# Performance work log

Measured on AMD Instinct MI355X. Metric: run time of the kernel, lower is better.

The kernel has to match this reference:

```python
import jax, jax.numpy as jnp
import numpy as np
import math

H = 128
NUM_RBF = 32
CUTOFF_UPPER = 4.5
CUTOFF_LOWER = 0.0
N_NODES = 16384
N_EDGES = 65536
EPS = 1e-5


def _layernorm(x, gamma, beta):
    m = x.mean(-1, keepdims=True)
    v = ((x - m) ** 2).mean(-1, keepdims=True)
    return (x - m) / jnp.sqrt(v + EPS) * gamma + beta


def _cosine_cutoff(d):
    # cutoff_lower == 0 branch of CosineCutoff
    return 0.5 * (jnp.cos(d * (math.pi / CUTOFF_UPPER)) + 1.0) * (d < CUTOFF_UPPER).astype(d.dtype)


def _expnorm_rbf(d):
    alpha = 5.0 / (CUTOFF_UPPER - CUTOFF_LOWER)
    start = math.exp(-CUTOFF_UPPER + CUTOFF_LOWER)
    means = jnp.linspace(start, 1.0, NUM_RBF, dtype=d.dtype)
    betas = jnp.full((NUM_RBF,), (2.0 / NUM_RBF * (1.0 - start)) ** -2, dtype=d.dtype)
    de = d[:, None]
    return _cosine_cutoff(de) * jnp.exp(-betas * (jnp.exp(alpha * (-de + CUTOFF_LOWER)) - means) ** 2)


def _skew(v):  # [E,3] -> [E,3,3]
    z = jnp.zeros(v.shape[0], v.dtype)
    return jnp.stack([z, -v[:, 2], v[:, 1], v[:, 2], z, -v[:, 0], -v[:, 1], v[:, 0], z], axis=1).reshape(-1, 3, 3)


def _sym(v):  # traceless symmetric part of outer product, [E,3] -> [E,3,3]
    M = v[:, :, None] * v[:, None, :]
    tr3 = (v * v).sum(-1)[:, None, None] / 3.0
    return M - tr3 * jnp.eye(3, dtype=v.dtype)


def _tensor_norm(T):  # [...,3,3] -> [...]
    return (T ** 2).sum((-2, -1))


def setup_inputs() -> dict:
    key = jax.random.key(0)
    ks = jax.random.split(key, 32)
    s = 0.05
    inp = {
        'z': jax.random.randint(ks[0], (N_NODES,), 0, 128, dtype=jnp.int32),
        'pos': jax.random.normal(ks[1], (N_NODES, 3), jnp.float32) * 3.0,
        'batch': jnp.zeros((N_NODES,), jnp.int32),
        'edge_index': jax.random.randint(ks[2], (2, N_EDGES), 0, N_NODES, dtype=jnp.int64),
        'emb_w': jax.random.normal(ks[3], (128, H), jnp.float32) * s,
        'emb2_w': jax.random.normal(ks[4], (H, 2 * H), jnp.float32) * s,
        'emb2_b': jnp.zeros((H,), jnp.float32),
        'dp1_w': jax.random.normal(ks[5], (H, NUM_RBF), jnp.float32) * s,
        'dp1_b': jnp.zeros((H,), jnp.float32),
        'dp2_w': jax.random.normal(ks[6], (H, NUM_RBF), jnp.float32) * s,
        'dp2_b': jnp.zeros((H,), jnp.float32),
        'dp3_w': jax.random.normal(ks[7], (H, NUM_RBF), jnp.float32) * s,
        'dp3_b': jnp.zeros((H,), jnp.float32),
        'lt0_w': jax.random.normal(ks[8], (H, H), jnp.float32) * s,
        'lt1_w': jax.random.normal(ks[9], (H, H), jnp.float32) * s,
        'lt2_w': jax.random.normal(ks[10], (H, H), jnp.float32) * s,
        'ls0_w': jax.random.normal(ks[11], (2 * H, H), jnp.float32) * s,
        'ls0_b': jnp.zeros((2 * H,), jnp.float32),
        'ls1_w': jax.random.normal(ks[12], (3 * H, 2 * H), jnp.float32) * s,
        'ls1_b': jnp.zeros((3 * H,), jnp.float32),
        'in_gamma': jnp.ones((H,), jnp.float32),
        'in_beta': jnp.zeros((H,), jnp.float32),
        'lin_w': jax.random.normal(ks[13], (H, 3 * H), jnp.float32) * s,
        'lin_b': jnp.zeros((H,), jnp.float32),
        'on_gamma': jnp.ones((3 * H,), jnp.float32),
        'on_beta': jnp.zeros((3 * H,), jnp.float32),
        'ol1_w': jax.random.normal(ks[14], (H // 2, H), jnp.float32) * s,
        'ol1_b': jnp.zeros((H // 2,), jnp.float32),
        'ol2_w': jax.random.normal(ks[15], (1, H // 2), jnp.float32) * s,
        'ol2_b': jnp.zeros((1,), jnp.float32),
    }
    return inp


def reference(z, pos, batch, edge_index, emb_w, emb2_w, emb2_b, dp1_w, dp1_b, dp2_w, dp2_b,
              dp3_w, dp3_b, lt0_w, lt1_w, lt2_w, ls0_w, ls0_b, ls1_w, ls1_b,
              in_gamma, in_beta, lin_w, lin_b, on_gamma, on_beta, ol1_w, ol1_b, ol2_w, ol2_b):
    src, dst = edge_index[0], edge_index[1]
    edge_vec = pos[src] - pos[dst]                            # [E,3]
    edge_weight = jnp.sqrt((edge_vec ** 2).sum(-1))           # [E]
    edge_attr = _expnorm_rbf(edge_weight)                     # [E,R]
    self_mask = src == dst
    edge_vec_norm = edge_vec / jnp.where(self_mask, 1.0, edge_weight)[:, None]

    # atomic-number message: Zij = emb2(concat(emb[z_src], emb[z_dst]))
    Zemb = emb_w[z]                                           # [N,H]
    Zcat = jnp.concatenate([Zemb[src], Zemb[dst]], axis=-1)   # [E,2H]
    Zij = Zcat @ emb2_w.T + emb2_b                            # [E,H]

    C = (_cosine_cutoff(edge_weight)[:, None] * Zij)[:, :, None, None]  # [E,H,1,1]
    eye = jnp.eye(3, dtype=pos.dtype)[None, None]
    d1 = (edge_attr @ dp1_w.T + dp1_b)[:, :, None, None]      # [E,H,1,1]
    d2 = (edge_attr @ dp2_w.T + dp2_b)[:, :, None, None]
    d3 = (edge_attr @ dp3_w.T + dp3_b)[:, :, None, None]
    Iij = d1 * C * eye                                        # [E,H,3,3]
    Aij = d2 * C * _skew(edge_vec_norm)[:, None, :, :]
    Sij = d3 * C * _sym(edge_vec_norm)[:, None, :, :]

    N = pos.shape[0]
    I0 = jax.ops.segment_sum(Iij, src, num_segments=N)        # [N,H,3,3]
    A0 = jax.ops.segment_sum(Aij, src, num_segments=N)
    S0 = jax.ops.segment_sum(Sij, src, num_segments=N)

    tnorm = _layernorm(_tensor_norm(I0 + A0 + S0), in_gamma, in_beta)  # [N,H]
    nrm = jax.nn.silu(tnorm @ ls0_w.T + ls0_b)
    nrm = jax.nn.silu(nrm @ ls1_w.T + ls1_b).reshape(-1, H, 3)          # [N,H,3]

    I = jnp.einsum('nhij,kh->nkij', I0, lt0_w) * nrm[:, :, 0, None, None]
    A = jnp.einsum('nhij,kh->nkij', A0, lt1_w) * nrm[:, :, 1, None, None]
    S = jnp.einsum('nhij,kh->nkij', S0, lt2_w) * nrm[:, :, 2, None, None]

    x = jnp.concatenate([_tensor_norm(I), _tensor_norm(A), _tensor_norm(S)], axis=-1)  # [N,3H]
    x = _layernorm(x, on_gamma, on_beta)
    x = jax.nn.silu(x @ lin_w.T + lin_b)                       # [N,H]
    x = jax.nn.silu(x @ ol1_w.T + ol1_b)                       # [N,H//2]
    y = x @ ol2_w.T + ol2_b                                    # [N,1] per-atom scalar
    return y
```

## Files before the change

### kernel.cpp

```cpp
#include <hip/hip_runtime.h>
#include <math.h>

#define NN 16384
#define NE 65536
#define HH 128

constexpr double D_START = 0.011108996538242306;
constexpr double D_STEP  = (1.0 - D_START) / 31.0;
constexpr float  F_ALPHA = (float)(5.0/4.5);
constexpr double D_BB    = (2.0/32.0)*(1.0 - D_START);
constexpr float  F_BETA  = (float)(1.0/(D_BB*D_BB));
constexpr float  F_PIC   = (float)(M_PI/4.5);

#define POOL_BYTES (16u*1024u*1024u)
__device__ __align__(256) static char g_pool[POOL_BYTES];

typedef __attribute__((ext_vector_type(8))) short bf16x8;
typedef __attribute__((ext_vector_type(4))) float f32x4;

__device__ __forceinline__ float siluf(float x){
  return x * (1.0f/(1.0f + expf(-x)));
}
__device__ __forceinline__ short f2bf(float x){
  unsigned u = __float_as_uint(x);
  unsigned r = (u + 0x7fffu + ((u>>16)&1u)) >> 16;
  return (short)r;
}
__device__ __forceinline__ float bf2f(short h){
  return __uint_as_float(((unsigned)(unsigned short)h)<<16);
}
__device__ __forceinline__ void split_bf(float x, short& h, short& l){
  h = f2bf(x);
  l = f2bf(x - bf2f(h));
}

__global__ __launch_bounds__(256) void k_prep(
    const int* __restrict__ ei, const float* __restrict__ pos,
    const int* __restrict__ z,
    const float* __restrict__ emb_w, const float* __restrict__ emb2_w,
    const float* __restrict__ emb2_b,
    const float* __restrict__ ls0, const float* __restrict__ ls1,
    const float* __restrict__ lin, const float* __restrict__ lt0,
    const float* __restrict__ lt1, const float* __restrict__ lt2,
    const float* __restrict__ dp1, const float* __restrict__ dp2,
    const float* __restrict__ dp3, const float* __restrict__ ol1,
    float* __restrict__ PZ, float* __restrict__ QZ,
    int* __restrict__ bcnt, int* __restrict__ bucket,
    int* __restrict__ ezs, int* __restrict__ ezd, float* __restrict__ ev,
    short* __restrict__ atth, short* __restrict__ attl,
    short* __restrict__ ls0h, short* __restrict__ ls0l,
    short* __restrict__ ls1h, short* __restrict__ ls1l,
    short* __restrict__ linh, short* __restrict__ linl,
    short* __restrict__ lt0h, short* __restrict__ lt0l,
    short* __restrict__ lt1h, short* __restrict__ lt1l,
    short* __restrict__ lt2h, short* __restrict__ lt2l,
    short* __restrict__ dwh, short* __restrict__ dwl,
    short* __restrict__ ol1h, short* __restrict__ ol1l){
  int b = blockIdx.x;
  if (b < 64){
    __shared__ float erow[2][128];
    int sub = threadIdx.x >> 7, h = threadIdx.x & 127;
    int a = b*2 + sub;
    erow[sub][h] = emb_w[a*128 + h];
    __syncthreads();
    float p = 0.f, q = 0.f;
    #pragma unroll 8
    for (int k=0;k<128;++k){
      float e = erow[sub][k];
      p += e * emb2_w[h*256 + k];
      q += e * emb2_w[h*256 + 128 + k];
    }
    PZ[a*128 + h] = p + emb2_b[h];
    QZ[a*128 + h] = q;
    return;
  }
  if (b < 1040){
    int tid = (b-64)*256 + threadIdx.x;
    const float* s; short *dh, *dl; int i;
    if      (tid < 32768)  { s=ls0; dh=ls0h; dl=ls0l; i=tid; }
    else if (tid < 131072) { s=ls1; dh=ls1h; dl=ls1l; i=tid-32768; }
    else if (tid < 180224) { s=lin; dh=linh; dl=linl; i=tid-131072; }
    else if (tid < 196608) { s=lt0; dh=lt0h; dl=lt0l; i=tid-180224; }
    else if (tid < 212992) { s=lt1; dh=lt1h; dl=lt1l; i=tid-196608; }
    else if (tid < 229376) { s=lt2; dh=lt2h; dl=lt2l; i=tid-212992; }
    else if (tid < 241664) {
      int j = tid - 229376;
      int g = j >> 12, idx = j & 4095;
      s = (g==0)?dp1:((g==1)?dp2:dp3);
      short h,l; split_bf(s[idx], h, l);
      dwh[j] = h; dwl[j] = l;
      return;
    }
    else { s=ol1; dh=ol1h; dl=ol1l; i=tid-241664; }
    short h,l; split_bf(s[i], h, l);
    dh[i] = h; dl[i] = l;
    return;
  }
  {
    int e = (b-1040)*256 + threadIdx.x;
    int s = ei[e];
    int t = ei[NE + e];
    float dx = pos[3*s+0] - pos[3*t+0];
    float dy = pos[3*s+1] - pos[3*t+1];
    float dz = pos[3*s+2] - pos[3*t+2];
    float d = sqrtf(dx*dx + dy*dy + dz*dz);
    if (d < 4.5f){
      int g16 = s >> 4;
      int p = atomicAdd(&bcnt[g16], 1);
      if (p < 512) bucket[g16*512 + p] = (e<<4) | (s & 15);
      ezs[e] = z[s];
      ezd[e] = z[t];
      float denom = (s==t) ? 1.0f : d;
      ev[4*e+0] = dx/denom;
      ev[4*e+1] = dy/denom;
      ev[4*e+2] = dz/denom;
      float cut = 0.5f*(cosf(d*F_PIC) + 1.0f);
      ev[4*e+3] = cut;
      float q = expf(-F_ALPHA*d);
      #pragma unroll
      for (int r=0;r<32;++r){
        float m = (float)(D_START + r*D_STEP);
        float u = q - m;
        float a = cut * expf(-F_BETA*u*u);
        short hh, ll; split_bf(a, hh, ll);
        atth[32*e + r] = hh;
        attl[32*e + r] = ll;
      }
    }
  }
}

__global__ __launch_bounds__(256, 2) void k_mega(
    const int* __restrict__ bcnt, const int* __restrict__ bucket,
    const int* __restrict__ ezs, const int* __restrict__ ezd,
    const float* __restrict__ ev,
    const short* __restrict__ atth, const short* __restrict__ attl,
    const short* __restrict__ dwh, const short* __restrict__ dwl,
    const float* __restrict__ db1, const float* __restrict__ db2,
    const float* __restrict__ db3,
    const float* __restrict__ PZ, const float* __restrict__ QZ,
    const float* __restrict__ in_g, const float* __restrict__ in_b,
    const short* __restrict__ w0h, const short* __restrict__ w0l,
    const short* __restrict__ w1h, const short* __restrict__ w1l,
    const short* __restrict__ w2h, const short* __restrict__ w2l,
    const short* __restrict__ ls0h, const short* __restrict__ ls0l,
    const float* __restrict__ ls0b,
    const short* __restrict__ ls1h, const short* __restrict__ ls1l,
    const float* __restrict__ ls1b,
    const short* __restrict__ linh, const short* __restrict__ linl,
    const float* __restrict__ linb,
    const short* __restrict__ ol1h, const short* __restrict__ ol1l,
    const float* __restrict__ ol1b,
    const float* __restrict__ ol2w, const float* __restrict__ ol2b,
    const float* __restrict__ on_g, const float* __restrict__ on_b,
    float* __restrict__ y){
  __shared__ __align__(16) char sm[76288];
  float* Dt    = (float*)sm;
  int*   elocal= (int*)(sm + 24832);
  int*   lcnt  = (int*)(sm + 26880);
  int*   loff  = lcnt + 16;
  int*   lcur  = loff + 17;
  short* T1h   = (short*)sm;
  short* T1l   = (short*)(sm + 9216);
  short* PlnL  = (short*)sm;
  float* xls   = (float*)sm;
  short* X3h   = (short*)sm;
  short* X3l   = (short*)(sm + 5120);
  float* partL = (float*)(sm + 10240);
  int*   tmpb  = (int*)(sm + 51200);
  short* tnhL  = (short*)(sm + 51200);
  short* tnlL  = (short*)(sm + 51200 + 5120);
  float* NRMt  = (float*)(sm + 51200);
  short* xhL   = (short*)(sm + 51200);
  short* xlL   = (short*)(sm + 51200 + 12544);

  int t = threadIdx.x;
  int b = blockIdx.x;
  int w = t >> 6, lane = t & 63;
  int col16 = lane & 15, quad = lane >> 4;
  int bn = b*16;
  int node = t >> 4, q = t & 15;

  int ecnt = bcnt[b]; if (ecnt > 512) ecnt = 512;
  if (t < 16){ lcnt[t] = 0; lcur[t] = 0; }
  __syncthreads();
  for (int j = t; j < ecnt; j += 256){
    int val = bucket[b*512 + j];
    tmpb[j] = val;
    atomicAdd(&lcnt[val & 15], 1);
  }
  __syncthreads();
  if (t == 0){
    int a = 0;
    #pragma unroll
    for (int i=0;i<16;++i){ loff[i] = a; a += lcnt[i]; }
    loff[16] = a;
  }
  __syncthreads();
  for (int j = t; j < ecnt; j += 256){
    int val = tmpb[j];
    int nd = val & 15;
    int p = loff[nd] + atomicAdd(&lcur[nd], 1);
    elocal[p] = val >> 4;
  }
  __syncthreads();
  int etot = loff[16];
  int e0n = loff[node], e1n = loff[node+1];

  float pv[10][8];
  #pragma unroll
  for (int p=0;p<10;++p)
    #pragma unroll
    for (int i=0;i<8;++i) pv[p][i]=0.f;

  const float* dbp[3] = {db1, db2, db3};
  for (int c0 = 0; c0 < etot; c0 += 16){
    int jA = c0 + col16; if (jA >= etot) jA = etot - 1;
    int eA = elocal[jA];
    bf16x8 ah = *(const bf16x8*)(atth + (size_t)eA*32 + quad*8);
    bf16x8 al = *(const bf16x8*)(attl + (size_t)eA*32 + quad*8);
    f32x4 dacc[6];
    #pragma unroll
    for (int nt=0;nt<6;++nt) dacc[nt] = (f32x4){0.f,0.f,0.f,0.f};
    #pragma unroll
    for (int nt=0;nt<6;++nt){
      int col = w*96 + nt*16 + col16;
      int g = col >> 7, cg = col & 127;
      bf16x8 wh = *(const bf16x8*)(dwh + g*4096 + cg*32 + quad*8);
      bf16x8 wl = *(const bf16x8*)(dwl + g*4096 + cg*32 + quad*8);
      dacc[nt] = __builtin_amdgcn_mfma_f32_16x16x32_bf16(ah, wh, dacc[nt], 0,0,0);
      dacc[nt] = __builtin_amdgcn_mfma_f32_16x16x32_bf16(ah, wl, dacc[nt], 0,0,0);
      dacc[nt] = __builtin_amdgcn_mfma_f32_16x16x32_bf16(al, wh, dacc[nt], 0,0,0);
    }
    #pragma unroll
    for (int nt=0;nt<6;++nt){
      int col = w*96 + nt*16 + col16;
      int g = col >> 7;
      float bb = dbp[g][col & 127];
      #pragma unroll
      for (int r=0;r<4;++r)
        Dt[(quad*4+r)*388 + col] = dacc[nt][r] + bb;
    }
    __syncthreads();
    int jlo = e0n > c0 ? e0n : c0;
    int jhi0 = c0 + 16; if (jhi0 > etot) jhi0 = etot;
    int jhi = e1n < jhi0 ? e1n : jhi0;
    for (int j = jlo; j < jhi; ++j){
      int le = j - c0;
      int e = elocal[j];
      float4 evv = *(const float4*)(ev + 4*e);
      int zs = ezs[e], zd = ezd[e];
      const float* pz = PZ + zs*128 + q*8;
      const float* qz = QZ + zd*128 + q*8;
      const float* dr = Dt + le*388 + q*8;
      float vx = evv.x, vy = evv.y, vz = evv.z, cut = evv.w;
      float t3v = (vx*vx + vy*vy + vz*vz)*(1.0f/3.0f);
      #pragma unroll
      for (int i=0;i<8;++i){
        float C = cut * (pz[i] + qz[i]);
        float d1 = dr[i], d2 = dr[128+i], d3 = dr[256+i];
        pv[0][i] += d1*C;
        float wa = d2*C;
        pv[1][i] += wa*vx; pv[2][i] += wa*vy; pv[3][i] += wa*vz;
        float ws = d3*C;
        pv[4][i] += ws*(vx*vx - t3v);
        pv[5][i] += ws*(vy*vy - t3v);
        pv[6][i] += ws*(vz*vz - t3v);
        pv[7][i] += ws*(vx*vy);
        pv[8][i] += ws*(vx*vz);
        pv[9][i] += ws*(vy*vz);
      }
    }
    __syncthreads();
  }

  {
    float tnv[8];
    float s8 = 0.f;
    #pragma unroll
    for (int i=0;i<8;++i){
      float x = 3.f*pv[0][i]*pv[0][i]
              + 2.f*(pv[1][i]*pv[1][i]+pv[2][i]*pv[2][i]+pv[3][i]*pv[3][i])
              + (pv[4][i]*pv[4][i]+pv[5][i]*pv[5][i]+pv[6][i]*pv[6][i])
              + 2.f*(pv[7][i]*pv[7][i]+pv[8][i]*pv[8][i]+pv[9][i]*pv[9][i]);
      tnv[i] = x; s8 += x;
    }
    #pragma unroll
    for (int o=8;o;o>>=1) s8 += __shfl_xor(s8, o, 64);
    float mean = s8*(1.0f/128.0f);
    float vq = 0.f;
    #pragma unroll
    for (int i=0;i<8;++i){ float d = tnv[i]-mean; vq += d*d; }
    #pragma unroll
    for (int o=8;o;o>>=1) vq += __shfl_xor(vq, o, 64);
    float rstd = 1.0f/sqrtf(vq*(1.0f/128.0f) + 1e-5f);
    #pragma unroll
    for (int i=0;i<8;++i){
      int h = q*8 + i;
      float val = (tnv[i]-mean)*rstd*in_g[h] + in_b[h];
      short hh, ll; split_bf(val, hh, ll);
      tnhL[node*160 + h] = hh;
      tnlL[node*160 + h] = ll;
    }
  }
  __syncthreads();

  {
    f32x4 macc[4];
    #pragma unroll
    for (int nt=0;nt<4;++nt) macc[nt] = (f32x4){0.f,0.f,0.f,0.f};
    #pragma unroll
    for (int kc=0; kc<4; ++kc){
      bf16x8 tah = *(const bf16x8*)(tnhL + col16*160 + kc*32 + quad*8);
      bf16x8 tal = *(const bf16x8*)(tnlL + col16*160 + kc*32 + quad*8);
      #pragma unroll
      for (int nt=0;nt<4;++nt){
        int n = w*64 + nt*16 + col16;
        bf16x8 wh = *(const bf16x8*)(ls0h + n*128 + kc*32 + quad*8);
        bf16x8 wl = *(const bf16x8*)(ls0l + n*128 + kc*32 + quad*8);
        macc[nt] = __builtin_amdgcn_mfma_f32_16x16x32_bf16(tah, wh, macc[nt], 0,0,0);
        macc[nt] = __builtin_amdgcn_mfma_f32_16x16x32_bf16(tah, wl, macc[nt], 0,0,0);
        macc[nt] = __builtin_amdgcn_mfma_f32_16x16x32_bf16(tal, wh, macc[nt], 0,0,0);
      }
    }
    #pragma unroll
    for (int nt=0;nt<4;++nt){
      int n = w*64 + nt*16 + col16;
      float bb = ls0b[n];
      #pragma unroll
      for (int r=0;r<4;++r){
        float v = siluf(macc[nt][r] + bb);
        short hh, ll; split_bf(v, hh, ll);
        T1h[(quad*4+r)*288 + n] = hh;
        T1l[(quad*4+r)*288 + n] = ll;
      }
    }
    __syncthreads();
    f32x4 nacc[6];
    #pragma unroll
    for (int nt=0;nt<6;++nt) nacc[nt] = (f32x4){0.f,0.f,0.f,0.f};
    #pragma unroll
    for (int kc=0; kc<8; ++kc){
      bf16x8 tah = *(const bf16x8*)(T1h + col16*288 + kc*32 + quad*8);
      bf16x8 tal = *(const bf16x8*)(T1l + col16*288 + kc*32 + quad*8);
      #pragma unroll
      for (int nt=0;nt<6;++nt){
        int n = w*96 + nt*16 + col16;
        bf16x8 wh = *(const bf16x8*)(ls1h + n*256 + kc*32 + quad*8);
        bf16x8 wl = *(const bf16x8*)(ls1l + n*256 + kc*32 + quad*8);
        nacc[nt] = __builtin_amdgcn_mfma_f32_16x16x32_bf16(tah, wh, nacc[nt], 0,0,0);
        nacc[nt] = __builtin_amdgcn_mfma_f32_16x16x32_bf16(tah, wl, nacc[nt], 0,0,0);
        nacc[nt] = __builtin_amdgcn_mfma_f32_16x16x32_bf16(tal, wh, nacc[nt], 0,0,0);
      }
    }
    __syncthreads();
    #pragma unroll
    for (int nt=0;nt<6;++nt){
      int n = w*96 + nt*16 + col16;
      float bb = ls1b[n];
      #pragma unroll
      for (int r=0;r<4;++r)
        NRMt[(quad*4+r)*388 + n] = siluf(nacc[nt][r] + bb);
    }
  }

  const short* wgh[3] = {w0h, w1h, w2h};
  const short* wgl[3] = {w0l, w1l, w2l};
  float xI[2][4], xA[2][4], xS[2][4];
  #pragma unroll
  for (int tt=0;tt<2;++tt)
    #pragma unroll
    for (int r=0;r<4;++r){ xI[tt][r]=0.f; xA[tt][r]=0.f; xS[tt][r]=0.f; }
  #pragma unroll
  for (int pass=0; pass<2; ++pass){
    const int pbase = pass*5;
    __syncthreads();
    #pragma unroll
    for (int pl=0; pl<5; ++pl){
      short* dst = PlnL + (pl*4 + (q>>2))*1280 + node*80 + (q&3)*16;
      #pragma unroll
      for (int i=0;i<8;++i){
        short hh, ll; split_bf(pv[pbase+pl][i], hh, ll);
        dst[i] = hh; dst[8+i] = ll;
      }
    }
    __syncthreads();
    f32x4 acc[5][2];
    #pragma unroll
    for (int pl=0;pl<5;++pl)
      #pragma unroll
      for (int tt=0;tt<2;++tt) acc[pl][tt] = (f32x4){0.f,0.f,0.f,0.f};
    #pragma unroll
    for (int hc4=0; hc4<4; ++hc4){
      bf16x8 bh[2], bl[2];
      int curg = -1;
      #pragma unroll
      for (int pl=0; pl<5; ++pl){
        const int p = pbase + pl;
        const int g = (p==0)?0:((p<4)?1:2);
        if (g != curg){
          #pragma unroll
          for (int tt=0; tt<2; ++tt){
            int row = w*32 + tt*16 + col16;
            bh[tt] = *(const bf16x8*)(wgh[g] + row*128 + hc4*32 + quad*8);
            bl[tt] = *(const bf16x8*)(wgl[g] + row*128 + hc4*32 + quad*8);
          }
          curg = g;
        }
        const short* ab = PlnL + (pl*4 + hc4)*1280 + col16*80 + quad*16;
        bf16x8 ah = *(const bf16x8*)(ab);
        bf16x8 al = *(const bf16x8*)(ab + 8);
        #pragma unroll
        for (int tt=0; tt<2; ++tt){
          acc[pl][tt] = __builtin_amdgcn_mfma_f32_16x16x32_bf16(ah, bh[tt], acc[pl][tt], 0,0,0);
          acc[pl][tt] = __builtin_amdgcn_mfma_f32_16x16x32_bf16(ah, bl[tt], acc[pl][tt], 0,0,0);
          acc[pl][tt] = __builtin_amdgcn_mfma_f32_16x16x32_bf16(al, bh[tt], acc[pl][tt], 0,0,0);
        }
      }
    }
    #pragma unroll
    for (int pl=0; pl<5; ++pl){
      const int p = pbase + pl;
      const int sel = (p==0)?0:((p<4)?1:2);
      #pragma unroll
      for (int tt=0; tt<2; ++tt){
        int k = w*32 + tt*16 + col16;
        #pragma unroll
        for (int r=0; r<4; ++r){
          int nloc = quad*4 + r;
          float n = NRMt[nloc*388 + 3*k + sel];
          float v = acc[pl][tt][r]*n;
          if (p==0)      xI[tt][r]  = 3.f*v*v;
          else if (p<4)  xA[tt][r] += 2.f*v*v;
          else if (p<7)  xS[tt][r] += v*v;
          else           xS[tt][r] += 2.f*v*v;
        }
      }
    }
  }
  __syncthreads();

  #pragma unroll
  for (int tt=0; tt<2; ++tt){
    int k = w*32 + tt*16 + col16;
    #pragma unroll
    for (int r=0; r<4; ++r){
      int nloc = quad*4 + r;
      xls[nloc*388 + k]       = xI[tt][r];
      xls[nloc*388 + 128 + k] = xA[tt][r];
      xls[nloc*388 + 256 + k] = xS[tt][r];
    }
  }
  __syncthreads();
  {
    float vv[24];
    float s = 0.f;
    #pragma unroll
    for (int i=0;i<24;++i){ vv[i] = xls[node*388 + q*24 + i]; s += vv[i]; }
    #pragma unroll
    for (int o=8;o;o>>=1) s += __shfl_xor(s, o, 64);
    float mean = s*(1.0f/384.0f);
    float qsum = 0.f;
    #pragma unroll
    for (int i=0;i<24;++i){ float d = vv[i]-mean; qsum += d*d; }
    #pragma unroll
    for (int o=8;o;o>>=1) qsum += __shfl_xor(qsum, o, 64);
    float rstd = 1.0f/sqrtf(qsum*(1.0f/384.0f) + 1e-5f);
    #pragma unroll
    for (int i=0;i<24;++i){
      int c = q*24 + i;
      float val = (vv[i]-mean)*rstd*on_g[c] + on_b[c];
      short hh, ll; split_bf(val, hh, ll);
      xhL[node*392 + c] = hh;
      xlL[node*392 + c] = ll;
    }
  }
  __syncthreads();

  {
    f32x4 lacc[2];
    #pragma unroll
    for (int nt=0;nt<2;++nt) lacc[nt] = (f32x4){0.f,0.f,0.f,0.f};
    #pragma unroll
    for (int kc=0; kc<12; ++kc){
      bf16x8 xah = *(const bf16x8*)(xhL + col16*392 + kc*32 + quad*8);
      bf16x8 xal = *(const bf16x8*)(xlL + col16*392 + kc*32 + quad*8);
      #pragma unroll
      for (int nt=0;nt<2;++nt){
        int n = w*32 + nt*16 + col16;
        bf16x8 wh = *(const bf16x8*)(linh + n*384 + kc*32 + quad*8);
        bf16x8 wl = *(const bf16x8*)(linl + n*384 + kc*32 + quad*8);
        lacc[nt] = __builtin_amdgcn_mfma_f32_16x16x32_bf16(xah, wh, lacc[nt], 0,0,0);
        lacc[nt] = __builtin_amdgcn_mfma_f32_16x16x32_bf16(xah, wl, lacc[nt], 0,0,0);
        lacc[nt] = __builtin_amdgcn_mfma_f32_16x16x32_bf16(xal, wh, lacc[nt], 0,0,0);
      }
    }
    __syncthreads();
    #pragma unroll
    for (int nt=0;nt<2;++nt){
      int n = w*32 + nt*16 + col16;
      float bb = linb[n];
      #pragma unroll
      for (int r=0;r<4;++r){
        float v = siluf(lacc[nt][r] + bb);
        short hh, ll; split_bf(v, hh, ll);
        X3h[(quad*4+r)*160 + n] = hh;
        X3l[(quad*4+r)*160 + n] = ll;
      }
    }
    __syncthreads();
  }

  {
    f32x4 hacc = (f32x4){0.f,0.f,0.f,0.f};
    int n = w*16 + col16;
    #pragma unroll
    for (int kc=0; kc<4; ++kc){
      bf16x8 xah = *(const bf16x8*)(X3h + col16*160 + kc*32 + quad*8);
      bf16x8 xal = *(const bf16x8*)(X3l + col16*160 + kc*32 + quad*8);
      bf16x8 wh = *(const bf16x8*)(ol1h + n*128 + kc*32 + quad*8);
      bf16x8 wl = *(const bf16x8*)(ol1l + n*128 + kc*32 + quad*8);
      hacc = __builtin_amdgcn_mfma_f32_16x16x32_bf16(xah, wh, hacc, 0,0,0);
      hacc = __builtin_amdgcn_mfma_f32_16x16x32_bf16(xah, wl, hacc, 0,0,0);
      hacc = __builtin_amdgcn_mfma_f32_16x16x32_bf16(xal, wh, hacc, 0,0,0);
    }
    float b1 = ol1b[n], w2 = ol2w[n];
    #pragma unroll
    for (int r=0;r<4;++r){
      float v = siluf(hacc[r] + b1) * w2;
      #pragma unroll
      for (int o=8;o;o>>=1) v += __shfl_xor(v, o, 64);
      if (col16 == 0) partL[w*16 + quad*4 + r] = v;
    }
    __syncthreads();
    if (t < 16)
      y[bn + t] = partL[t] + partL[16+t] + partL[32+t] + partL[48+t] + ol2b[0];
  }
}

extern "C" void kernel_launch(void* const* d_in, const int* in_sizes, int n_in,
                              void* d_out, int out_size, void* d_ws, size_t ws_size,
                              hipStream_t stream) {
  const int*   z      = (const int*)d_in[0];
  const float* pos    = (const float*)d_in[1];
  const int*   ei     = (const int*)d_in[3];
  const float* emb_w  = (const float*)d_in[4];
  const float* emb2_w = (const float*)d_in[5];
  const float* emb2_b = (const float*)d_in[6];
  const float* dp1_w  = (const float*)d_in[7];
  const float* dp1_b  = (const float*)d_in[8];
  const float* dp2_w  = (const float*)d_in[9];
  const float* dp2_b  = (const float*)d_in[10];
  const float* dp3_w  = (const float*)d_in[11];
  const float* dp3_b  = (const float*)d_in[12];
  const float* lt0_w  = (const float*)d_in[13];
  const float* lt1_w  = (const float*)d_in[14];
  const float* lt2_w  = (const float*)d_in[15];
  const float* ls0_w  = (const float*)d_in[16];
  const float* ls0_b  = (const float*)d_in[17];
  const float* ls1_w  = (const float*)d_in[18];
  const float* ls1_b  = (const float*)d_in[19];
  const float* in_g   = (const float*)d_in[20];
  const float* in_b   = (const float*)d_in[21];
  const float* lin_w  = (const float*)d_in[22];
  const float* lin_b  = (const float*)d_in[23];
  const float* on_g   = (const float*)d_in[24];
  const float* on_b   = (const float*)d_in[25];
  const float* ol1_w  = (const float*)d_in[26];
  const float* ol1_b  = (const float*)d_in[27];
  const float* ol2_w  = (const float*)d_in[28];
  const float* ol2_b  = (const float*)d_in[29];
  float* out = (float*)d_out;

  const size_t NEED = 14u*1024u*1024u;
  char* wsb = (char*)d_ws;
  if (ws_size < NEED){
    void* p = nullptr;
    hipGetSymbolAddress(&p, HIP_SYMBOL(g_pool));
    wsb = (char*)p;
  }
  size_t off = 0;
  auto alloc = [&](size_t bytes)->void*{
    void* p = wsb + off;
    off = (off + bytes + 255) & ~(size_t)255;
    return p;
  };
  float* PZ      = (float*)alloc(128*128*4);
  float* QZ      = (float*)alloc(128*128*4);
  int*   bcnt    = (int*)  alloc(1024*4);
  int*   bucket  = (int*)  alloc((size_t)1024*512*4);
  int*   ezs     = (int*)  alloc(NE*4);
  int*   ezd     = (int*)  alloc(NE*4);
  float* ev      = (float*)alloc((size_t)NE*4*4);
  short* atth    = (short*)alloc((size_t)NE*32*2);
  short* attl    = (short*)alloc((size_t)NE*32*2);
  short* dwh     = (short*)alloc(3*128*32*2);
  short* dwl     = (short*)alloc(3*128*32*2);
  short* ls0h    = (short*)alloc(256*128*2);
  short* ls0l    = (short*)alloc(256*128*2);
  short* ls1h    = (short*)alloc(384*256*2);
  short* ls1l    = (short*)alloc(384*256*2);
  short* linh    = (short*)alloc(128*384*2);
  short* linl    = (short*)alloc(128*384*2);
  short* lt0h    = (short*)alloc(128*128*2);
  short* lt0l    = (short*)alloc(128*128*2);
  short* lt1h    = (short*)alloc(128*128*2);
  short* lt1l    = (short*)alloc(128*128*2);
  short* lt2h    = (short*)alloc(128*128*2);
  short* lt2l    = (short*)alloc(128*128*2);
  short* ol1h    = (short*)alloc(64*128*2);
  short* ol1l    = (short*)alloc(64*128*2);

  hipMemsetAsync(bcnt, 0, 1024*4, stream);

  k_prep<<<1296, 256, 0, stream>>>(ei, pos, z, emb_w, emb2_w, emb2_b,
                                   ls0_w, ls1_w, lin_w, lt0_w, lt1_w, lt2_w,
                                   dp1_w, dp2_w, dp3_w, ol1_w,
                                   PZ, QZ, bcnt, bucket, ezs, ezd, ev, atth, attl,
                                   ls0h, ls0l, ls1h, ls1l, linh, linl,
                                   lt0h, lt0l, lt1h, lt1l, lt2h, lt2l,
                                   dwh, dwl, ol1h, ol1l);
  k_mega<<<NN/16, 256, 0, stream>>>(bcnt, bucket, ezs, ezd, ev, atth, attl,
                                    dwh, dwl, dp1_b, dp2_b, dp3_b,
                                    PZ, QZ, in_g, in_b,
                                    lt0h, lt0l, lt1h, lt1l, lt2h, lt2l,
                                    ls0h, ls0l, ls0_b, ls1h, ls1l, ls1_b,
                                    linh, linl, lin_b, ol1h, ol1l, ol1_b,
                                    ol2_w, ol2_b, on_g, on_b, out);
}
```

Baseline: 266.9 us.

## Double k_mega block size to 512 threads, halving per-thread work

Raises the fused per-node kernel from 256 to 512 threads per block (8 waves), with 32 threads per node each owning 4 hidden channels instead of 8. All MFMA tile loops are re-split so each wave handles half as many output tiles. The aim is fewer registers per thread and more waves to hide the latency of gathers and MFMAs. The cost is more barrier participants, wider shuffle reductions, and possible LDS pressure limiting the requested 4 blocks per CU.

Result: no change. 264.8 us (median of 2 runs) (-0.8%).

```diff
diff --git a/kernel.cpp b/kernel.cpp
--- a/kernel.cpp
+++ b/kernel.cpp
@@ -130,7 +130,7 @@
   }
 }
 
-__global__ __launch_bounds__(256, 2) void k_mega(
+__global__ __launch_bounds__(512, 4) void k_mega(
     const int* __restrict__ bcnt, const int* __restrict__ bucket,
     const int* __restrict__ ezs, const int* __restrict__ ezd,
     const float* __restrict__ ev,
@@ -179,12 +179,12 @@
   int w = t >> 6, lane = t & 63;
   int col16 = lane & 15, quad = lane >> 4;
   int bn = b*16;
-  int node = t >> 4, q = t & 15;
+  int node = t >> 5, q5 = t & 31;
 
   int ecnt = bcnt[b]; if (ecnt > 512) ecnt = 512;
   if (t < 16){ lcnt[t] = 0; lcur[t] = 0; }
   __syncthreads();
-  for (int j = t; j < ecnt; j += 256){
+  for (int j = t; j < ecnt; j += 512){
     int val = bucket[b*512 + j];
     tmpb[j] = val;
     atomicAdd(&lcnt[val & 15], 1);
@@ -197,7 +197,7 @@
     loff[16] = a;
   }
   __syncthreads();
-  for (int j = t; j < ecnt; j += 256){
+  for (int j = t; j < ecnt; j += 512){
     int val = tmpb[j];
     int nd = val & 15;
     int p = loff[nd] + atomicAdd(&lcur[nd], 1);
@@ -207,11 +207,11 @@
   int etot = loff[16];
   int e0n = loff[node], e1n = loff[node+1];
 
-  float pv[10][8];
+  float pv[10][4];
   #pragma unroll
   for (int p=0;p<10;++p)
     #pragma unroll
-    for (int i=0;i<8;++i) pv[p][i]=0.f;
+    for (int i=0;i<4;++i) pv[p][i]=0.f;
 
   const float* dbp[3] = {db1, db2, db3};
   for (int c0 = 0; c0 < etot; c0 += 16){
@@ -219,12 +219,12 @@
     int eA = elocal[jA];
     bf16x8 ah = *(const bf16x8*)(atth + (size_t)eA*32 + quad*8);
     bf16x8 al = *(const bf16x8*)(attl + (size_t)eA*32 + quad*8);
-    f32x4 dacc[6];
-    #pragma unroll
-    for (int nt=0;nt<6;++nt) dacc[nt] = (f32x4){0.f,0.f,0.f,0.f};
-    #pragma unroll
-    for (int nt=0;nt<6;++nt){
-      int col = w*96 + nt*16 + col16;
+    f32x4 dacc[3];
+    #pragma unroll
+    for (int nt=0;nt<3;++nt) dacc[nt] = (f32x4){0.f,0.f,0.f,0.f};
+    #pragma unroll
+    for (int nt=0;nt<3;++nt){
+      int col = w*48 + nt*16 + col16;
       int g = col >> 7, cg = col & 127;
       bf16x8 wh = *(const bf16x8*)(dwh + g*4096 + cg*32 + quad*8);
       bf16x8 wl = *(const bf16x8*)(dwl + g*4096 + cg*32 + quad*8);
@@ -233,8 +233,8 @@
       dacc[nt] = __builtin_amdgcn_mfma_f32_16x16x32_bf16(al, wh, dacc[nt], 0,0,0);
     }
     #pragma unroll
-    for (int nt=0;nt<6;++nt){
-      int col = w*96 + nt*16 + col16;
+    for (int nt=0;nt<3;++nt){
+      int col = w*48 + nt*16 + col16;
       int g = col >> 7;
       float bb = dbp[g][col & 127];
       #pragma unroll
@@ -245,18 +245,19 @@
     int jlo = e0n > c0 ? e0n : c0;
     int jhi0 = c0 + 16; if (jhi0 > etot) jhi0 = etot;
     int jhi = e1n < jhi0 ? e1n : jhi0;
+    int h0 = q5*4;
     for (int j = jlo; j < jhi; ++j){
       int le = j - c0;
       int e = elocal[j];
       float4 evv = *(const float4*)(ev + 4*e);
       int zs = ezs[e], zd = ezd[e];
-      const float* pz = PZ + zs*128 + q*8;
-      const float* qz = QZ + zd*128 + q*8;
-      const float* dr = Dt + le*388 + q*8;
+      const float* pz = PZ + zs*128 + h0;
+      const float* qz = QZ + zd*128 + h0;
+      const float* dr = Dt + le*388 + h0;
       float vx = evv.x, vy = evv.y, vz = evv.z, cut = evv.w;
       float t3v = (vx*vx + vy*vy + vz*vz)*(1.0f/3.0f);
       #pragma unroll
-      for (int i=0;i<8;++i){
+      for (int i=0;i<4;++i){
         float C = cut * (pz[i] + qz[i]);
         float d1 = dr[i], d2 = dr[128+i], d3 = dr[256+i];
         pv[0][i] += d1*C;
@@ -275,10 +276,10 @@
   }
 
   {
-    float tnv[8];
+    float tnv[4];
     float s8 = 0.f;
     #pragma unroll
-    for (int i=0;i<8;++i){
+    for (int i=0;i<4;++i){
       float x = 3.f*pv[0][i]*pv[0][i]
               + 2.f*(pv[1][i]*pv[1][i]+pv[2][i]*pv[2][i]+pv[3][i]*pv[3][i])
               + (pv[4][i]*pv[4][i]+pv[5][i]*pv[5][i]+pv[6][i]*pv[6][i])
@@ -286,17 +287,17 @@
       tnv[i] = x; s8 += x;
     }
     #pragma unroll
-    for (int o=8;o;o>>=1) s8 += __shfl_xor(s8, o, 64);
+    for (int o=16;o;o>>=1) s8 += __shfl_xor(s8, o, 64);
     float mean = s8*(1.0f/128.0f);
     float vq = 0.f;
     #pragma unroll
-    for (int i=0;i<8;++i){ float d = tnv[i]-mean; vq += d*d; }
-    #pragma unroll
-    for (int o=8;o;o>>=1) vq += __shfl_xor(vq, o, 64);
+    for (int i=0;i<4;++i){ float d = tnv[i]-mean; vq += d*d; }
+    #pragma unroll
+    for (int o=16;o;o>>=1) vq += __shfl_xor(vq, o, 64);
     float rstd = 1.0f/sqrtf(vq*(1.0f/128.0f) + 1e-5f);
     #pragma unroll
-    for (int i=0;i<8;++i){
-      int h = q*8 + i;
+    for (int i=0;i<4;++i){
+      int h = q5*4 + i;
       float val = (tnv[i]-mean)*rstd*in_g[h] + in_b[h];
       short hh, ll; split_bf(val, hh, ll);
       tnhL[node*160 + h] = hh;
@@ -306,16 +307,16 @@
   __syncthreads();
 
   {
-    f32x4 macc[4];
-    #pragma unroll
-    for (int nt=0;nt<4;++nt) macc[nt] = (f32x4){0.f,0.f,0.f,0.f};
+    f32x4 macc[2];
+    #pragma unroll
+    for (int nt=0;nt<2;++nt) macc[nt] = (f32x4){0.f,0.f,0.f,0.f};
     #pragma unroll
     for (int kc=0; kc<4; ++kc){
       bf16x8 tah = *(const bf16x8*)(tnhL + col16*160 + kc*32 + quad*8);
       bf16x8 tal = *(const bf16x8*)(tnlL + col16*160 + kc*32 + quad*8);
       #pragma unroll
-      for (int nt=0;nt<4;++nt){
-        int n = w*64 + nt*16 + col16;
+      for (int nt=0;nt<2;++nt){
+        int n = w*32 + nt*16 + col16;
         bf16x8 wh = *(const bf16x8*)(ls0h + n*128 + kc*32 + quad*8);
         bf16x8 wl = *(const bf16x8*)(ls0l + n*128 + kc*32 + quad*8);
         macc[nt] = __builtin_amdgcn_mfma_f32_16x16x32_bf16(tah, wh, macc[nt], 0,0,0);
@@ -324,8 +325,8 @@
       }
     }
     #pragma unroll
-    for (int nt=0;nt<4;++nt){
-      int n = w*64 + nt*16 + col16;
+    for (int nt=0;nt<2;++nt){
+      int n = w*32 + nt*16 + col16;
       float bb = ls0b[n];
       #pragma unroll
       for (int r=0;r<4;++r){
@@ -336,16 +337,16 @@
       }
     }
     __syncthreads();
-    f32x4 nacc[6];
-    #pragma unroll
-    for (int nt=0;nt<6;++nt) nacc[nt] = (f32x4){0.f,0.f,0.f,0.f};
+    f32x4 nacc[3];
+    #pragma unroll
+    for (int nt=0;nt<3;++nt) nacc[nt] = (f32x4){0.f,0.f,0.f,0.f};
     #pragma unroll
     for (int kc=0; kc<8; ++kc){
       bf16x8 tah = *(const bf16x8*)(T1h + col16*288 + kc*32 + quad*8);
       bf16x8 tal = *(const bf16x8*)(T1l + col16*288 + kc*32 + quad*8);
       #pragma unroll
-      for (int nt=0;nt<6;++nt){
-        int n = w*96 + nt*16 + col16;
+      for (int nt=0;nt<3;++nt){
+        int n = w*48 + nt*16 + col16;
         bf16x8 wh = *(const bf16x8*)(ls1h + n*256 + kc*32 + quad*8);
         bf16x8 wl = *(const bf16x8*)(ls1l + n*256 + kc*32 + quad*8);
         nacc[nt] = __builtin_amdgcn_mfma_f32_16x16x32_bf16(tah, wh, nacc[nt], 0,0,0);
@@ -355,8 +356,8 @@
     }
     __syncthreads();
     #pragma unroll
-    for (int nt=0;nt<6;++nt){
-      int n = w*96 + nt*16 + col16;
+    for (int nt=0;nt<3;++nt){
+      int n = w*48 + nt*16 + col16;
       float bb = ls1b[n];
       #pragma unroll
       for (int r=0;r<4;++r)
@@ -366,109 +367,95 @@
 
   const short* wgh[3] = {w0h, w1h, w2h};
   const short* wgl[3] = {w0l, w1l, w2l};
-  float xI[2][4], xA[2][4], xS[2][4];
+  float xI[4], xA[4], xS[4];
   #pragma unroll
-  for (int tt=0;tt<2;++tt)
-    #pragma unroll
-    for (int r=0;r<4;++r){ xI[tt][r]=0.f; xA[tt][r]=0.f; xS[tt][r]=0.f; }
+  for (int r=0;r<4;++r){ xI[r]=0.f; xA[r]=0.f; xS[r]=0.f; }
   #pragma unroll
   for (int pass=0; pass<2; ++pass){
     const int pbase = pass*5;
     __syncthreads();
     #pragma unroll
     for (int pl=0; pl<5; ++pl){
-      short* dst = PlnL + (pl*4 + (q>>2))*1280 + node*80 + (q&3)*16;
-      #pragma unroll
-      for (int i=0;i<8;++i){
+      short* dst = PlnL + (pl*4 + (q5>>3))*1280 + node*80 + ((q5>>1)&3)*16 + (q5&1)*4;
+      #pragma unroll
+      for (int i=0;i<4;++i){
         short hh, ll; split_bf(pv[pbase+pl][i], hh, ll);
         dst[i] = hh; dst[8+i] = ll;
       }
     }
     __syncthreads();
-    f32x4 acc[5][2];
-    #pragma unroll
-    for (int pl=0;pl<5;++pl)
-      #pragma unroll
-      for (int tt=0;tt<2;++tt) acc[pl][tt] = (f32x4){0.f,0.f,0.f,0.f};
+    f32x4 acc[5];
+    #pragma unroll
+    for (int pl=0;pl<5;++pl) acc[pl] = (f32x4){0.f,0.f,0.f,0.f};
     #pragma unroll
     for (int hc4=0; hc4<4; ++hc4){
-      bf16x8 bh[2], bl[2];
+      bf16x8 bh, bl;
       int curg = -1;
       #pragma unroll
       for (int pl=0; pl<5; ++pl){
         const int p = pbase + pl;
         const int g = (p==0)?0:((p<4)?1:2);
         if (g != curg){
-          #pragma unroll
-          for (int tt=0; tt<2; ++tt){
-            int row = w*32 + tt*16 + col16;
-            bh[tt] = *(const bf16x8*)(wgh[g] + row*128 + hc4*32 + quad*8);
-            bl[tt] = *(const bf16x8*)(wgl[g] + row*128 + hc4*32 + quad*8);
-          }
+          int row = w*16 + col16;
+          bh = *(const bf16x8*)(wgh[g] + row*128 + hc4*32 + quad*8);
+          bl = *(const bf16x8*)(wgl[g] + row*128 + hc4*32 + quad*8);
           curg = g;
         }
         const short* ab = PlnL + (pl*4 + hc4)*1280 + col16*80 + quad*16;
         bf16x8 ah = *(const bf16x8*)(ab);
         bf16x8 al = *(const bf16x8*)(ab + 8);
-        #pragma unroll
-        for (int tt=0; tt<2; ++tt){
-          acc[pl][tt] = __builtin_amdgcn_mfma_f32_16x16x32_bf16(ah, bh[tt], acc[pl][tt], 0,0,0);
-          acc[pl][tt] = __builtin_amdgcn_mfma_f32_16x16x32_bf16(ah, bl[tt], acc[pl][tt], 0,0,0);
-          acc[pl][tt] = __builtin_amdgcn_mfma_f32_16x16x32_bf16(al, bh[tt], acc[pl][tt], 0,0,0);
-        }
+        acc[pl] = __builtin_amdgcn_mfma_f32_16x16x32_bf16(ah, bh, acc[pl], 0,0,0);
+        acc[pl] = __builtin_amdgcn_mfma_f32_16x16x32_bf16(ah, bl, acc[pl], 0,0,0);
+        acc[pl] = __builtin_amdgcn_mfma_f32_16x16x32_bf16(al, bh, acc[pl], 0,0,0);
       }
     }
     #pragma unroll
     for (int pl=0; pl<5; ++pl){
       const int p = pbase + pl;
       const int sel = (p==0)?0:((p<4)?1:2);
-      #pragma unroll
-      for (int tt=0; tt<2; ++tt){
-        int k = w*32 + tt*16 + col16;
-        #pragma unroll
-        for (int r=0; r<4; ++r){
-          int nloc = quad*4 + r;
-          float n = NRMt[nloc*388 + 3*k + sel];
-          float v = acc[pl][tt][r]*n;
-          if (p==0)      xI[tt][r]  = 3.f*v*v;
-          else if (p<4)  xA[tt][r] += 2.f*v*v;
-          else if (p<7)  xS[tt][r] += v*v;
-          else           xS[tt][r] += 2.f*v*v;
-        }
-      }
-    }
-  }
-  __syncthreads();
-
-  #pragma unroll
-  for (int tt=0; tt<2; ++tt){
-    int k = w*32 + tt*16 + col16;
+      int k = w*16 + col16;
+      #pragma unroll
+      for (int r=0; r<4; ++r){
+        int nloc = quad*4 + r;
+        float n = NRMt[nloc*388 + 3*k + sel];
+        float v = acc[pl][r]*n;
+        if (p==0)      xI[r]  = 3.f*v*v;
+        else if (p<4)  xA[r] += 2.f*v*v;
+        else if (p<7)  xS[r] += v*v;
+        else           xS[r] += 2.f*v*v;
+      }
+    }
+  }
+  __syncthreads();
+
+  {
+    int k = w*16 + col16;
     #pragma unroll
     for (int r=0; r<4; ++r){
       int nloc = quad*4 + r;
-      xls[nloc*388 + k]       = xI[tt][r];
-      xls[nloc*388 + 128 + k] = xA[tt][r];
-      xls[nloc*388 + 256 + k] = xS[tt][r];
+      xls[nloc*388 + k]       = xI[r];
+      xls[nloc*388 + 128 + k] = xA[r];
+      xls[nloc*388 + 256 + k] = xS[r];
     }
   }
   __syncthreads();
   {
-    float vv[24];
+    float vv[12];
     float s = 0.f;
     #pragma unroll
-    for (int i=0;i<24;++i){ vv[i] = xls[node*388 + q*24 + i]; s += vv[i]; }
-    #pragma unroll
-    for (int o=8;o;o>>=1) s += __shfl_xor(s, o, 64);
+    for (int i=0;i<12;++i){ vv[i] = xls[node*388 + q5*12 + i]; s += vv[i]; }
+    #pragma unroll
+    for (int o=16;o;o>>=1) s += __shfl_xor(s, o, 64);
     float mean = s*(1.0f/384.0f);
     float qsum = 0.f;
     #pragma unroll
-    for (int i=0;i<24;++i){ float d = vv[i]-mean; qsum += d*d; }
-    #pragma unroll
-    for (int o=8;o;o>>=1) qsum += __shfl_xor(qsum, o, 64);
+    for (int i=0;i<12;++i){ float d = vv[i]-mean; qsum += d*d; }
+    #pragma unroll
+    for (int o=16;o;o>>=1) qsum += __shfl_xor(qsum, o, 64);
     float rstd = 1.0f/sqrtf(qsum*(1.0f/384.0f) + 1e-5f);
     #pragma unroll
-    for (int i=0;i<24;++i){
-      int c = q*24 + i;
+    for (int i=0;i<12;++i){
+      int c = q5*12 + i;
       float val = (vv[i]-mean)*rstd*on_g[c] + on_b[c];
       short hh, ll; split_bf(val, hh, ll);
       xhL[node*392 + c] = hh;
@@ -478,40 +465,31 @@
   __syncthreads();
 
   {
-    f32x4 lacc[2];
-    #pragma unroll
-    for (int nt=0;nt<2;++nt) lacc[nt] = (f32x4){0.f,0.f,0.f,0.f};
+    f32x4 lacc = (f32x4){0.f,0.f,0.f,0.f};
+    int n = w*16 + col16;
     #pragma unroll
     for (int kc=0; kc<12; ++kc){
       bf16x8 xah = *(const bf16x8*)(xhL + col16*392 + kc*32 + quad*8);
       bf16x8 xal = *(const bf16x8*)(xlL + col16*392 + kc*32 + quad*8);
-      #pragma unroll
-      for (int nt=0;nt<2;++nt){
-        int n = w*32 + nt*16 + col16;
-        bf16x8 wh = *(const bf16x8*)(linh + n*384 + kc*32 + quad*8);
-        bf16x8 wl = *(const bf16x8*)(linl + n*384 + kc*32 + quad*8);
-        lacc[nt] = __builtin_amdgcn_mfma_f32_16x16x32_bf16(xah, wh, lacc[nt], 0,0,0);
-        lacc[nt] = __builtin_amdgcn_mfma_f32_16x16x32_bf16(xah, wl, lacc[nt], 0,0,0);
-        lacc[nt] = __builtin_amdgcn_mfma_f32_16x16x32_bf16(xal, wh, lacc[nt], 0,0,0);
-      }
-    }
-    __syncthreads();
-    #pragma unroll
-    for (int nt=0;nt<2;++nt){
-      int n = w*32 + nt*16 + col16;
-      float bb = linb[n];
-      #pragma unroll
-      for (int r=0;r<4;++r){
-        float v = siluf(lacc[nt][r] + bb);
-        short hh, ll; split_bf(v, hh, ll);
-        X3h[(quad*4+r)*160 + n] = hh;
-        X3l[(quad*4+r)*160 + n] = ll;
-      }
-    }
-    __syncthreads();
-  }
-
-  {
+      bf16x8 wh = *(const bf16x8*)(linh + n*384 + kc*32 + quad*8);
+      bf16x8 wl = *(const bf16x8*)(linl + n*384 + kc*32 + quad*8);
+      lacc = __builtin_amdgcn_mfma_f32_16x16x32_bf16(xah, wh, lacc, 0,0,0);
+      lacc = __builtin_amdgcn_mfma_f32_16x16x32_bf16(xah, wl, lacc, 0,0,0);
+      lacc = __builtin_amdgcn_mfma_f32_16x16x32_bf16(xal, wh, lacc, 0,0,0);
+    }
+    __syncthreads();
+    float bb = linb[n];
+    #pragma unroll
+    for (int r=0;r<4;++r){
+      float v = siluf(lacc[r] + bb);
+      short hh, ll; split_bf(v, hh, ll);
+      X3h[(quad*4+r)*160 + n] = hh;
+      X3l[(quad*4+r)*160 + n] = ll;
+    }
+    __syncthreads();
+  }
+
+  if (w < 4){
     f32x4 hacc = (f32x4){0.f,0.f,0.f,0.f};
     int n = w*16 + col16;
     #pragma unroll
@@ -532,10 +510,10 @@
       for (int o=8;o;o>>=1) v += __shfl_xor(v, o, 64);
       if (col16 == 0) partL[w*16 + quad*4 + r] = v;
     }
-    __syncthreads();
-    if (t < 16)
-      y[bn + t] = partL[t] + partL[16+t] + partL[32+t] + partL[48+t] + ol2b[0];
-  }
+  }
+  __syncthreads();
+  if (t < 16)
+    y[bn + t] = partL[t] + partL[16+t] + partL[32+t] + partL[48+t] + ol2b[0];
 }
 
 extern "C" void kernel_launch(void* const* d_in, const int* in_sizes, int n_in,
@@ -620,7 +598,7 @@
                                    ls0h, ls0l, ls1h, ls1l, linh, linl,
                                    lt0h, lt0l, lt1h, lt1l, lt2h, lt2l,
                                    dwh, dwl, ol1h, ol1l);
-  k_mega<<<NN/16, 256, 0, stream>>>(bcnt, bucket, ezs, ezd, ev, atth, attl,
+  k_mega<<<NN/16, 512, 0, stream>>>(bcnt, bucket, ezs, ezd, ev, atth, attl,
                                     dwh, dwl, dp1_b, dp2_b, dp3_b,
                                     PZ, QZ, in_g, in_b,
                                     lt0h, lt0l, lt1h, lt1l, lt2h, lt2l,
```

## Recompute per-edge geometry and RBF inside mega kernel instead of materialising

Applied to the files above, without the earlier changes.

Moves the per-edge vector, cutoff, atomic-number lookup and 32-term RBF expansion out of the prep kernel and into the mega kernel. There they are computed per 16-edge chunk into shared memory. This removes the global writes and reads of the ev, ezs, ezd and bf16 hi/lo RBF arrays. In exchange it adds two block-wide barriers per chunk, and the serial per-chunk geometry work runs on only 16 threads.

After: 268.0 us. Within noise of the previous version (+0.4%).

```diff
diff --git a/kernel.cpp b/kernel.cpp
--- a/kernel.cpp
+++ b/kernel.cpp
@@ -12,7 +12,7 @@
 constexpr float  F_BETA  = (float)(1.0/(D_BB*D_BB));
 constexpr float  F_PIC   = (float)(M_PI/4.5);
 
-#define POOL_BYTES (16u*1024u*1024u)
+#define POOL_BYTES (8u*1024u*1024u)
 __device__ __align__(256) static char g_pool[POOL_BYTES];
 
 typedef __attribute__((ext_vector_type(8))) short bf16x8;
@@ -36,7 +36,6 @@
 
 __global__ __launch_bounds__(256) void k_prep(
     const int* __restrict__ ei, const float* __restrict__ pos,
-    const int* __restrict__ z,
     const float* __restrict__ emb_w, const float* __restrict__ emb2_w,
     const float* __restrict__ emb2_b,
     const float* __restrict__ ls0, const float* __restrict__ ls1,
@@ -46,8 +45,6 @@
     const float* __restrict__ dp3, const float* __restrict__ ol1,
     float* __restrict__ PZ, float* __restrict__ QZ,
     int* __restrict__ bcnt, int* __restrict__ bucket,
-    int* __restrict__ ezs, int* __restrict__ ezd, float* __restrict__ ev,
-    short* __restrict__ atth, short* __restrict__ attl,
     short* __restrict__ ls0h, short* __restrict__ ls0l,
     short* __restrict__ ls1h, short* __restrict__ ls1l,
     short* __restrict__ linh, short* __restrict__ linl,
@@ -108,33 +105,14 @@
       int g16 = s >> 4;
       int p = atomicAdd(&bcnt[g16], 1);
       if (p < 512) bucket[g16*512 + p] = (e<<4) | (s & 15);
-      ezs[e] = z[s];
-      ezd[e] = z[t];
-      float denom = (s==t) ? 1.0f : d;
-      ev[4*e+0] = dx/denom;
-      ev[4*e+1] = dy/denom;
-      ev[4*e+2] = dz/denom;
-      float cut = 0.5f*(cosf(d*F_PIC) + 1.0f);
-      ev[4*e+3] = cut;
-      float q = expf(-F_ALPHA*d);
-      #pragma unroll
-      for (int r=0;r<32;++r){
-        float m = (float)(D_START + r*D_STEP);
-        float u = q - m;
-        float a = cut * expf(-F_BETA*u*u);
-        short hh, ll; split_bf(a, hh, ll);
-        atth[32*e + r] = hh;
-        attl[32*e + r] = ll;
-      }
     }
   }
 }
 
 __global__ __launch_bounds__(256, 2) void k_mega(
     const int* __restrict__ bcnt, const int* __restrict__ bucket,
-    const int* __restrict__ ezs, const int* __restrict__ ezd,
-    const float* __restrict__ ev,
-    const short* __restrict__ atth, const short* __restrict__ attl,
+    const int* __restrict__ ei, const float* __restrict__ pos,
+    const int* __restrict__ zA,
     const short* __restrict__ dwh, const short* __restrict__ dwl,
     const float* __restrict__ db1, const float* __restrict__ db2,
     const float* __restrict__ db3,
@@ -167,12 +145,19 @@
   short* X3h   = (short*)sm;
   short* X3l   = (short*)(sm + 5120);
   float* partL = (float*)(sm + 10240);
-  int*   tmpb  = (int*)(sm + 51200);
-  short* tnhL  = (short*)(sm + 51200);
-  short* tnlL  = (short*)(sm + 51200 + 5120);
-  float* NRMt  = (float*)(sm + 51200);
-  short* xhL   = (short*)(sm + 51200);
-  short* xlL   = (short*)(sm + 51200 + 12544);
+  char*  Bb    = sm + 51200;
+  int*   tmpb  = (int*)Bb;
+  float4* evL  = (float4*)Bb;
+  float* qL    = (float*)(Bb + 256);
+  int*   zsL   = (int*)(Bb + 320);
+  int*   zdL   = (int*)(Bb + 384);
+  short* attH  = (short*)(Bb + 448);
+  short* attL2 = (short*)(Bb + 1472);
+  short* tnhL  = (short*)Bb;
+  short* tnlL  = (short*)(Bb + 5120);
+  float* NRMt  = (float*)Bb;
+  short* xhL   = (short*)Bb;
+  short* xlL   = (short*)(Bb + 12544);
 
   int t = threadIdx.x;
   int b = blockIdx.x;
@@ -215,10 +200,36 @@
 
   const float* dbp[3] = {db1, db2, db3};
   for (int c0 = 0; c0 < etot; c0 += 16){
-    int jA = c0 + col16; if (jA >= etot) jA = etot - 1;
-    int eA = elocal[jA];
-    bf16x8 ah = *(const bf16x8*)(atth + (size_t)eA*32 + quad*8);
-    bf16x8 al = *(const bf16x8*)(attl + (size_t)eA*32 + quad*8);
+    if (t < 16){
+      int j = c0 + t; if (j >= etot) j = etot - 1;
+      int e = elocal[j];
+      int s = ei[e], tt2 = ei[NE + e];
+      float dx = pos[3*s+0] - pos[3*tt2+0];
+      float dy = pos[3*s+1] - pos[3*tt2+1];
+      float dz = pos[3*s+2] - pos[3*tt2+2];
+      float d = sqrtf(dx*dx + dy*dy + dz*dz);
+      float denom = (s==tt2) ? 1.0f : d;
+      float cut = 0.5f*(cosf(d*F_PIC) + 1.0f);
+      evL[t] = make_float4(dx/denom, dy/denom, dz/denom, cut);
+      qL[t] = expf(-F_ALPHA*d);
+      zsL[t] = zA[s];
+      zdL[t] = zA[tt2];
+    }
+    __syncthreads();
+    #pragma unroll
+    for (int it=0; it<2; ++it){
+      int idx = t + it*256;
+      int le = idx >> 5, r = idx & 31;
+      float m = (float)(D_START + r*D_STEP);
+      float u = qL[le] - m;
+      float a = evL[le].w * expf(-F_BETA*u*u);
+      short hh, ll; split_bf(a, hh, ll);
+      attH[le*32 + r]  = hh;
+      attL2[le*32 + r] = ll;
+    }
+    __syncthreads();
+    bf16x8 ah = *(const bf16x8*)(attH  + col16*32 + quad*8);
+    bf16x8 al = *(const bf16x8*)(attL2 + col16*32 + quad*8);
     f32x4 dacc[6];
     #pragma unroll
     for (int nt=0;nt<6;++nt) dacc[nt] = (f32x4){0.f,0.f,0.f,0.f};
@@ -247,9 +258,8 @@
     int jhi = e1n < jhi0 ? e1n : jhi0;
     for (int j = jlo; j < jhi; ++j){
       int le = j - c0;
-      int e = elocal[j];
-      float4 evv = *(const float4*)(ev + 4*e);
-      int zs = ezs[e], zd = ezd[e];
+      float4 evv = evL[le];
+      int zs = zsL[le], zd = zdL[le];
       const float* pz = PZ + zs*128 + q*8;
       const float* qz = QZ + zd*128 + q*8;
       const float* dr = Dt + le*388 + q*8;
@@ -572,7 +582,7 @@
   const float* ol2_b  = (const float*)d_in[29];
   float* out = (float*)d_out;
 
-  const size_t NEED = 14u*1024u*1024u;
+  const size_t NEED = 4u*1024u*1024u;
   char* wsb = (char*)d_ws;
   if (ws_size < NEED){
     void* p = nullptr;
@@ -589,11 +599,6 @@
   float* QZ      = (float*)alloc(128*128*4);
   int*   bcnt    = (int*)  alloc(1024*4);
   int*   bucket  = (int*)  alloc((size_t)1024*512*4);
-  int*   ezs     = (int*)  alloc(NE*4);
-  int*   ezd     = (int*)  alloc(NE*4);
-  float* ev      = (float*)alloc((size_t)NE*4*4);
-  short* atth    = (short*)alloc((size_t)NE*32*2);
-  short* attl    = (short*)alloc((size_t)NE*32*2);
   short* dwh     = (short*)alloc(3*128*32*2);
   short* dwl     = (short*)alloc(3*128*32*2);
   short* ls0h    = (short*)alloc(256*128*2);
@@ -613,14 +618,14 @@
 
   hipMemsetAsync(bcnt, 0, 1024*4, stream);
 
-  k_prep<<<1296, 256, 0, stream>>>(ei, pos, z, emb_w, emb2_w, emb2_b,
+  k_prep<<<1296, 256, 0, stream>>>(ei, pos, emb_w, emb2_w, emb2_b,
                                    ls0_w, ls1_w, lin_w, lt0_w, lt1_w, lt2_w,
                                    dp1_w, dp2_w, dp3_w, ol1_w,
-                                   PZ, QZ, bcnt, bucket, ezs, ezd, ev, atth, attl,
+                                   PZ, QZ, bcnt, bucket,
                                    ls0h, ls0l, ls1h, ls1l, linh, linl,
                                    lt0h, lt0l, lt1h, lt1l, lt2h, lt2l,
                                    dwh, dwl, ol1h, ol1l);
-  k_mega<<<NN/16, 256, 0, stream>>>(bcnt, bucket, ezs, ezd, ev, atth, attl,
+  k_mega<<<NN/16, 256, 0, stream>>>(bcnt, bucket, ei, pos, z,
                                     dwh, dwl, dp1_b, dp2_b, dp3_b,
                                     PZ, QZ, in_g, in_b,
                                     lt0h, lt0l, lt1h, lt1l, lt2h, lt2l,
```
